# Kernel optimization log

Hardware: AMD Instinct MI355X
Metric: run time of the kernel (lower is better)

Reference implementation:

```python
import jax, jax.numpy as jnp
import numpy as np

N, D_IN, D_OUT, A, B = 100000, 128, 64, 8, 512
F = 2 * D_OUT  # feature_dim = output_dim * 2


def setup_inputs() -> dict:
    key = jax.random.key(0)
    ks = jax.random.split(key, 6)
    x = jax.random.normal(ks[0], (N, D_IN), jnp.float32)
    batch = jnp.sort(jax.random.randint(ks[1], (N,), 0, B)).astype(jnp.int32)
    def lin(k, out_d, in_d):
        return jax.random.normal(k, (out_d, in_d), jnp.float32) / np.float32(np.sqrt(in_d))
    W_in = lin(ks[2], F, D_IN)
    b_in = jnp.zeros((F,), jnp.float32)
    W_a = lin(ks[3], A, F)
    b_a = jnp.zeros((A,), jnp.float32)
    h_dim = 2 * F * A + D_IN + F
    W_out = lin(ks[4], D_OUT, h_dim)
    b_out = jnp.zeros((D_OUT,), jnp.float32)
    return {"x": x, "batch": batch, "num_segments": B,
            "W_in": W_in, "b_in": b_in, "W_a": W_a, "b_a": b_a,
            "W_out": W_out, "b_out": b_out}


def reference(x, batch, num_segments, W_in, b_in, W_a, b_a, W_out, b_out):
    # transform_in
    xp = x @ W_in.T + b_in                          # [N, F]
    # aggregator_activation('potential') = exp(-|.|)
    score = jnp.exp(-jnp.abs(xp @ W_a.T + b_a))     # [N, A]
    # einsum('nf,na->afn') materialized as [N, A, F] (node-major for segment ops)
    e = score[:, :, None] * xp[:, None, :]          # [N, A, F]
    seg_sum = jax.ops.segment_sum(e, batch, num_segments=num_segments)      # [B, A, F]
    counts = jax.ops.segment_sum(jnp.ones((e.shape[0], 1, 1), e.dtype), batch,
                                 num_segments=num_segments)                  # [B, 1, 1]
    mean_p = seg_sum / jnp.maximum(counts, 1.0)
    max_p = jax.ops.segment_max(e, batch, num_segments=num_segments)        # [B, A, F]
    max_p = jnp.where(counts > 0, max_p, 0.0)
    # cat along feature dim then flatten (A, 2F) -> matches torch transpose+cat+reshape
    agg = jnp.concatenate([mean_p, max_p], axis=-1).reshape(num_segments, -1)  # [B, 2*F*A]
    H = jnp.concatenate([x, xp, agg[batch]], axis=-1)  # [N, D_IN + F + 2*F*A]
    return jax.nn.relu(H @ W_out.T + b_out)            # [N, D_OUT]
```

## Files before the change

### kernel.cpp

```cpp
#include <hip/hip_runtime.h>
#include <math.h>

#define N_NODES 100000
#define D_INPUT 128
#define FDIM 128
#define A_HEADS 8
#define B_SEGS 512
#define D_OUTPUT 64
#define H_DIM 2304

typedef __attribute__((ext_vector_type(8))) __bf16 bf16x8;
typedef __attribute__((ext_vector_type(4))) float f32x4;

static __device__ inline unsigned short f2bfu(float f) {
    unsigned u = __builtin_bit_cast(unsigned, f);
    u += 0x7fffu + ((u >> 16) & 1u);
    return (unsigned short)(u >> 16);
}
static __device__ inline unsigned packbf(float a, float b) {
    return (unsigned)f2bfu(a) | ((unsigned)f2bfu(b) << 16);
}
static __device__ inline float bfl(unsigned u) {
    unsigned x = u << 16; return __builtin_bit_cast(float, x);
}
static __device__ inline float bfh(unsigned u) {
    unsigned x = u & 0xffff0000u; return __builtin_bit_cast(float, x);
}
static __device__ inline bf16x8 pack8(float4 a, float4 b) {
    union { unsigned u[4]; bf16x8 v; } r;
    r.u[0] = packbf(a.x, a.y); r.u[1] = packbf(a.z, a.w);
    r.u[2] = packbf(b.x, b.y); r.u[3] = packbf(b.z, b.w);
    return r.v;
}

__global__ void seg_bounds_kernel(const int* __restrict__ batch, int n,
                                  int* __restrict__ seg_start) {
    int b = threadIdx.x;
    if (b > B_SEGS) return;
    int lo = 0, hi = n;
    while (lo < hi) {
        int mid = (lo + hi) >> 1;
        if (batch[mid] < b) lo = mid + 1; else hi = mid;
    }
    seg_start[b] = lo;
}

__global__ __launch_bounds__(512, 2) void mega_kernel(
        const float* __restrict__ x, const int* __restrict__ seg_start,
        const float* __restrict__ W_in, const float* __restrict__ b_in,
        const float* __restrict__ W_a, const float* __restrict__ b_a,
        const float* __restrict__ W_out, const float* __restrict__ b_out,
        unsigned short* __restrict__ out_part, float* __restrict__ agg_proj) {
    __shared__ __align__(16) unsigned WbL[128 * 68];
    __shared__ __align__(16) unsigned WoL[64 * 132];
    __shared__ __align__(16) unsigned WaL[16 * 68];
    __shared__ __align__(16) unsigned XP[128 * 68];
    __shared__ float scoref[128 * 8];
    unsigned short* XPs = (unsigned short*)XP;
    float* XPf = (float*)XP;

    const int b = blockIdx.x;
    const int start = seg_start[b], end = seg_start[b + 1];
    const int cnt = end - start;
    const int t = threadIdx.x;

    if (cnt == 0) {
        if (t < 64) agg_proj[b * 64 + t] = b_out[t];
        return;
    }

#pragma unroll
    for (int i = 0; i < 16; ++i) {
        int idx = i * 512 + t, row = idx >> 6, c = idx & 63;
        float2 v = *(const float2*)(W_in + (size_t)row * 128 + c * 2);
        WbL[row * 68 + c] = packbf(v.x, v.y);
    }
#pragma unroll
    for (int i = 0; i < 16; ++i) {
        int idx = i * 512 + t, row = idx >> 7, c = idx & 127;
        float2 v = *(const float2*)(W_out + (size_t)row * H_DIM + c * 2);
        WoL[row * 132 + c] = packbf(v.x, v.y);
    }
    {
        int row = t >> 6, c = t & 63;
        float2 v = *(const float2*)(W_a + (size_t)row * 128 + c * 2);
        WaL[row * 68 + c] = packbf(v.x, v.y);
        WaL[(row + 8) * 68 + c] = 0u;
    }
    __syncthreads();

    const int w = t >> 6, l = t & 63, lr = l & 15, lk = l >> 4;
    const int a0 = t >> 6;
    const int f2 = t & 63;

    const f32x4 z4 = {0.f, 0.f, 0.f, 0.f};
    float sum0 = 0.f, sum1 = 0.f, mx0 = -INFINITY, mx1 = -INFINITY;

    for (int c0 = start; c0 < end; c0 += 128) {
        const int rc = min(128, end - c0);
        const int arow = c0 + w * 16 + lr;
        const int arowc = min(arow, end - 1);

        bf16x8 af[4];
#pragma unroll
        for (int ks = 0; ks < 4; ++ks) {
            const float4* xp4 = (const float4*)(x + (size_t)arowc * 128 + ks * 32 + lk * 8);
            af[ks] = pack8(xp4[0], xp4[1]);
        }
        f32x4 acc[8];
#pragma unroll
        for (int nr = 0; nr < 8; ++nr) acc[nr] = z4;
#pragma unroll
        for (int ks = 0; ks < 4; ++ks)
#pragma unroll
            for (int nr = 0; nr < 8; ++nr) {
                bf16x8 bfrag = *(const bf16x8*)&WbL[(nr * 16 + lr) * 68 + ks * 16 + lk * 4];
                acc[nr] = __builtin_amdgcn_mfma_f32_16x16x32_bf16(af[ks], bfrag, acc[nr], 0, 0, 0);
            }
#pragma unroll
        for (int nr = 0; nr < 8; ++nr) {
            float bf = b_in[nr * 16 + lr];
#pragma unroll
            for (int r = 0; r < 4; ++r) {
                int row = w * 16 + lk * 4 + r;
                XPs[row * 136 + nr * 16 + lr] = f2bfu(((const float*)&acc[nr])[r] + bf);
            }
        }
        bf16x8 xf[4];
#pragma unroll
        for (int ks = 0; ks < 4; ++ks)
            xf[ks] = *(const bf16x8*)&XPs[(w * 16 + lr) * 136 + ks * 32 + lk * 8];
        f32x4 sacc = z4;
#pragma unroll
        for (int ks = 0; ks < 4; ++ks) {
            bf16x8 bfrag = *(const bf16x8*)&WaL[lr * 68 + ks * 16 + lk * 4];
            sacc = __builtin_amdgcn_mfma_f32_16x16x32_bf16(xf[ks], bfrag, sacc, 0, 0, 0);
        }
        if (lr < A_HEADS) {
            float ba = b_a[lr];
#pragma unroll
            for (int r = 0; r < 4; ++r) {
                int row = w * 16 + lk * 4 + r;
                scoref[row * 8 + lr] = __expf(-fabsf(((const float*)&sacc)[r] + ba));
            }
        }
        f32x4 aco[4];
#pragma unroll
        for (int nr = 0; nr < 4; ++nr) aco[nr] = z4;
#pragma unroll
        for (int ks = 0; ks < 4; ++ks)
#pragma unroll
            for (int nr = 0; nr < 4; ++nr) {
                bf16x8 b0 = *(const bf16x8*)&WoL[(nr * 16 + lr) * 132 + ks * 16 + lk * 4];
                aco[nr] = __builtin_amdgcn_mfma_f32_16x16x32_bf16(af[ks], b0, aco[nr], 0, 0, 0);
                bf16x8 b1 = *(const bf16x8*)&WoL[(nr * 16 + lr) * 132 + 64 + ks * 16 + lk * 4];
                aco[nr] = __builtin_amdgcn_mfma_f32_16x16x32_bf16(xf[ks], b1, aco[nr], 0, 0, 0);
            }
#pragma unroll
        for (int nr = 0; nr < 4; ++nr)
#pragma unroll
            for (int r = 0; r < 4; ++r) {
                int n = c0 + w * 16 + lk * 4 + r;
                if (n < end)
                    out_part[(size_t)n * 64 + nr * 16 + lr] = f2bfu(((const float*)&aco[nr])[r]);
            }
        __syncthreads();

        for (int i = 0; i < rc; ++i) {
            unsigned u = XP[i * 68 + f2];
            float sa = scoref[i * 8 + a0];
            float e0 = sa * bfl(u), e1 = sa * bfh(u);
            sum0 += e0; sum1 += e1;
            mx0 = fmaxf(mx0, e0); mx1 = fmaxf(mx1, e1);
        }
        __syncthreads();
    }

    const float inv = 1.f / (float)cnt;
    XPf[a0 * 256 + 2 * f2]       = sum0 * inv;
    XPf[a0 * 256 + 2 * f2 + 1]   = sum1 * inv;
    XPf[a0 * 256 + 128 + 2 * f2]     = mx0;
    XPf[a0 * 256 + 128 + 2 * f2 + 1] = mx1;
    __syncthreads();

#pragma unroll
    for (int i = 0; i < 8; ++i) {
        int o = w * 8 + i;
        const float* wrow = W_out + (size_t)o * H_DIM + 256;
        float partial = 0.f;
#pragma unroll
        for (int c = 0; c < 8; ++c) {
            int jj = c * 256 + l * 4;
            float4 wv = *(const float4*)&wrow[jj];
            float4 av = *(const float4*)&XPf[jj];
            partial = fmaf(wv.x, av.x, partial);
            partial = fmaf(wv.y, av.y, partial);
            partial = fmaf(wv.z, av.z, partial);
            partial = fmaf(wv.w, av.w, partial);
        }
#pragma unroll
        for (int m = 1; m < 64; m <<= 1) partial += __shfl_xor(partial, m);
        if (l == 0) agg_proj[b * D_OUTPUT + o] = partial + b_out[o];
    }
}

__global__ __launch_bounds__(256) void out_final_kernel(
        const unsigned* __restrict__ out_part, const int* __restrict__ batch,
        const float* __restrict__ agg_proj, float* __restrict__ out) {
    int q = blockIdx.x * 256 + threadIdx.x;
    if (q >= N_NODES * 16) return;
    int n = q >> 4, c4 = (q & 15) * 4;
    int bs = batch[n];
    uint2 v = *(const uint2*)(out_part + (size_t)n * 32 + (c4 >> 1));
    float4 ap = *(const float4*)(agg_proj + (size_t)bs * 64 + c4);
    float4 o;
    o.x = fmaxf(bfl(v.x) + ap.x, 0.f);
    o.y = fmaxf(bfh(v.x) + ap.y, 0.f);
    o.z = fmaxf(bfl(v.y) + ap.z, 0.f);
    o.w = fmaxf(bfh(v.y) + ap.w, 0.f);
    *(float4*)(out + (size_t)n * 64 + c4) = o;
}

extern "C" void kernel_launch(void* const* d_in, const int* in_sizes, int n_in,
                              void* d_out, int out_size, void* d_ws, size_t ws_size,
                              hipStream_t stream) {
    const float* x     = (const float*)d_in[0];
    const int*   batch = (const int*)d_in[1];
    const float* W_in  = (const float*)d_in[3];
    const float* b_in  = (const float*)d_in[4];
    const float* W_a   = (const float*)d_in[5];
    const float* b_a   = (const float*)d_in[6];
    const float* W_out = (const float*)d_in[7];
    const float* b_out = (const float*)d_in[8];
    float* out = (float*)d_out;

    float* agg_proj = (float*)d_ws;
    int* seg_start = (int*)(agg_proj + B_SEGS * D_OUTPUT);
    unsigned short* out_part = (unsigned short*)(seg_start + 520);
    unsigned* out_part_u32 = (unsigned*)out_part;

    seg_bounds_kernel<<<1, 1024, 0, stream>>>(batch, N_NODES, seg_start);
    mega_kernel<<<B_SEGS, 512, 0, stream>>>(
        x, seg_start, W_in, b_in, W_a, b_a, W_out, b_out, out_part, agg_proj);
    out_final_kernel<<<(N_NODES * 16 + 255) / 256, 256, 0, stream>>>(
        out_part_u32, batch, agg_proj, out);
}
```

Baseline: 71.87 us.

## Split segments across two blocks, pre-convert weights, move aggregation projection to separate kernel

Weight bf16 conversion moves into a one-time prepass kernel, so the main kernel reads bf16 weight fragments straight from global/L2 instead of staging them in LDS. Each segment is now handled by two 256-thread blocks that write partial sum/max buffers. A new kernel combines the halves and projects the aggregate through bf16 W_out weights. The inner aggregation loop is unrolled by two, with each thread covering two heads. This raises parallelism and cuts LDS use, at the cost of extra launches, partial-buffer traffic, and weight fragment loads from global memory inside the MFMA loop.

```diff
diff --git a/kernel.cpp b/kernel.cpp
--- a/kernel.cpp
+++ b/kernel.cpp
@@ -45,61 +45,71 @@
     seg_start[b] = lo;
 }
 
-__global__ __launch_bounds__(512, 2) void mega_kernel(
+__global__ __launch_bounds__(256) void wconv_kernel(
+        const float* __restrict__ W_in, const float* __restrict__ W_a,
+        const float* __restrict__ W_out, unsigned* __restrict__ Wb,
+        unsigned* __restrict__ Wa, unsigned* __restrict__ Wo,
+        unsigned* __restrict__ Wagg) {
+    int i = blockIdx.x * 256 + threadIdx.x;
+    if (i < 8192) {
+        float2 v = *(const float2*)(W_in + (size_t)i * 2);
+        Wb[i] = packbf(v.x, v.y);
+    } else if (i < 9216) {
+        int j = i - 8192;
+        if (j < 512) {
+            float2 v = *(const float2*)(W_a + (size_t)j * 2);
+            Wa[j] = packbf(v.x, v.y);
+        } else Wa[j] = 0u;
+    } else if (i < 17408) {
+        int j = i - 9216;
+        int row = j >> 7, cu = j & 127;
+        float2 v = *(const float2*)(W_out + (size_t)row * H_DIM + cu * 2);
+        Wo[j] = packbf(v.x, v.y);
+    } else if (i < 82944) {
+        int j = i - 17408;
+        int row = j >> 10, cu = j & 1023;
+        float2 v = *(const float2*)(W_out + (size_t)row * H_DIM + 256 + cu * 2);
+        Wagg[j] = packbf(v.x, v.y);
+    }
+}
+
+__global__ __launch_bounds__(256, 4) void mega_kernel(
         const float* __restrict__ x, const int* __restrict__ seg_start,
-        const float* __restrict__ W_in, const float* __restrict__ b_in,
-        const float* __restrict__ W_a, const float* __restrict__ b_a,
-        const float* __restrict__ W_out, const float* __restrict__ b_out,
-        unsigned short* __restrict__ out_part, float* __restrict__ agg_proj) {
-    __shared__ __align__(16) unsigned WbL[128 * 68];
-    __shared__ __align__(16) unsigned WoL[64 * 132];
-    __shared__ __align__(16) unsigned WaL[16 * 68];
-    __shared__ __align__(16) unsigned XP[128 * 68];
-    __shared__ float scoref[128 * 8];
+        const float* __restrict__ b_in, const float* __restrict__ b_a,
+        const unsigned* __restrict__ Wb, const unsigned* __restrict__ Wa,
+        const unsigned* __restrict__ Wo, unsigned short* __restrict__ out_part,
+        float* __restrict__ psum, float* __restrict__ pmax) {
+    __shared__ __align__(16) unsigned XP[64 * 68];
+    __shared__ float scoref[64 * 8];
     unsigned short* XPs = (unsigned short*)XP;
-    float* XPf = (float*)XP;
-
-    const int b = blockIdx.x;
-    const int start = seg_start[b], end = seg_start[b + 1];
-    const int cnt = end - start;
+
+    const int bb = blockIdx.x;
+    const int seg = bb >> 1, half = bb & 1;
+    const int s0 = seg_start[seg], s1 = seg_start[seg + 1];
+    const int cnt = s1 - s0;
+    const int h = (cnt + 1) >> 1;
+    const int hstart = s0 + half * h;
+    const int hend = min(s1, hstart + h);
+
     const int t = threadIdx.x;
-
-    if (cnt == 0) {
-        if (t < 64) agg_proj[b * 64 + t] = b_out[t];
-        return;
-    }
-
-#pragma unroll
-    for (int i = 0; i < 16; ++i) {
-        int idx = i * 512 + t, row = idx >> 6, c = idx & 63;
-        float2 v = *(const float2*)(W_in + (size_t)row * 128 + c * 2);
-        WbL[row * 68 + c] = packbf(v.x, v.y);
-    }
-#pragma unroll
-    for (int i = 0; i < 16; ++i) {
-        int idx = i * 512 + t, row = idx >> 7, c = idx & 127;
-        float2 v = *(const float2*)(W_out + (size_t)row * H_DIM + c * 2);
-        WoL[row * 132 + c] = packbf(v.x, v.y);
-    }
-    {
-        int row = t >> 6, c = t & 63;
-        float2 v = *(const float2*)(W_a + (size_t)row * 128 + c * 2);
-        WaL[row * 68 + c] = packbf(v.x, v.y);
-        WaL[(row + 8) * 68 + c] = 0u;
-    }
-    __syncthreads();
-
     const int w = t >> 6, l = t & 63, lr = l & 15, lk = l >> 4;
-    const int a0 = t >> 6;
-    const int f2 = t & 63;
+    const int a0 = t >> 6, f2 = t & 63;
+
+    float binv[8];
+#pragma unroll
+    for (int nr = 0; nr < 8; ++nr) binv[nr] = b_in[nr * 16 + lr];
+    const float ba = b_a[lr & 7];
 
     const f32x4 z4 = {0.f, 0.f, 0.f, 0.f};
-    float sum0 = 0.f, sum1 = 0.f, mx0 = -INFINITY, mx1 = -INFINITY;
-
-    for (int c0 = start; c0 < end; c0 += 128) {
-        const int rc = min(128, end - c0);
+    float sum0a = 0.f, sum1a = 0.f, sum2a = 0.f, sum3a = 0.f;
+    float sum0b = 0.f, sum1b = 0.f, sum2b = 0.f, sum3b = 0.f;
+    float mx0a = -INFINITY, mx1a = -INFINITY, mx2a = -INFINITY, mx3a = -INFINITY;
+    float mx0b = -INFINITY, mx1b = -INFINITY, mx2b = -INFINITY, mx3b = -INFINITY;
+
+    for (int c0 = hstart; c0 < hend; c0 += 64) {
+        const int rc = min(64, hend - c0);
         const int arow = c0 + w * 16 + lr;
-        const int arowc = min(arow, end - 1);
+        const int arowc = min(arow, hend - 1);
 
         bf16x8 af[4];
 #pragma unroll
@@ -114,18 +124,16 @@
         for (int ks = 0; ks < 4; ++ks)
 #pragma unroll
             for (int nr = 0; nr < 8; ++nr) {
-                bf16x8 bfrag = *(const bf16x8*)&WbL[(nr * 16 + lr) * 68 + ks * 16 + lk * 4];
+                bf16x8 bfrag = *(const bf16x8*)&Wb[(nr * 16 + lr) * 64 + ks * 16 + lk * 4];
                 acc[nr] = __builtin_amdgcn_mfma_f32_16x16x32_bf16(af[ks], bfrag, acc[nr], 0, 0, 0);
             }
 #pragma unroll
-        for (int nr = 0; nr < 8; ++nr) {
-            float bf = b_in[nr * 16 + lr];
+        for (int nr = 0; nr < 8; ++nr)
 #pragma unroll
             for (int r = 0; r < 4; ++r) {
                 int row = w * 16 + lk * 4 + r;
-                XPs[row * 136 + nr * 16 + lr] = f2bfu(((const float*)&acc[nr])[r] + bf);
-            }
-        }
+                XPs[row * 136 + nr * 16 + lr] = f2bfu(((const float*)&acc[nr])[r] + binv[nr]);
+            }
         bf16x8 xf[4];
 #pragma unroll
         for (int ks = 0; ks < 4; ++ks)
@@ -133,11 +141,10 @@
         f32x4 sacc = z4;
 #pragma unroll
         for (int ks = 0; ks < 4; ++ks) {
-            bf16x8 bfrag = *(const bf16x8*)&WaL[lr * 68 + ks * 16 + lk * 4];
+            bf16x8 bfrag = *(const bf16x8*)&Wa[lr * 64 + ks * 16 + lk * 4];
             sacc = __builtin_amdgcn_mfma_f32_16x16x32_bf16(xf[ks], bfrag, sacc, 0, 0, 0);
         }
         if (lr < A_HEADS) {
-            float ba = b_a[lr];
 #pragma unroll
             for (int r = 0; r < 4; ++r) {
                 int row = w * 16 + lk * 4 + r;
@@ -151,9 +158,9 @@
         for (int ks = 0; ks < 4; ++ks)
 #pragma unroll
             for (int nr = 0; nr < 4; ++nr) {
-                bf16x8 b0 = *(const bf16x8*)&WoL[(nr * 16 + lr) * 132 + ks * 16 + lk * 4];
+                bf16x8 b0 = *(const bf16x8*)&Wo[(nr * 16 + lr) * 128 + ks * 16 + lk * 4];
                 aco[nr] = __builtin_amdgcn_mfma_f32_16x16x32_bf16(af[ks], b0, aco[nr], 0, 0, 0);
-                bf16x8 b1 = *(const bf16x8*)&WoL[(nr * 16 + lr) * 132 + 64 + ks * 16 + lk * 4];
+                bf16x8 b1 = *(const bf16x8*)&Wo[(nr * 16 + lr) * 128 + 64 + ks * 16 + lk * 4];
                 aco[nr] = __builtin_amdgcn_mfma_f32_16x16x32_bf16(xf[ks], b1, aco[nr], 0, 0, 0);
             }
 #pragma unroll
@@ -161,46 +168,91 @@
 #pragma unroll
             for (int r = 0; r < 4; ++r) {
                 int n = c0 + w * 16 + lk * 4 + r;
-                if (n < end)
+                if (n < hend)
                     out_part[(size_t)n * 64 + nr * 16 + lr] = f2bfu(((const float*)&aco[nr])[r]);
             }
         __syncthreads();
 
-        for (int i = 0; i < rc; ++i) {
-            unsigned u = XP[i * 68 + f2];
-            float sa = scoref[i * 8 + a0];
-            float e0 = sa * bfl(u), e1 = sa * bfh(u);
-            sum0 += e0; sum1 += e1;
-            mx0 = fmaxf(mx0, e0); mx1 = fmaxf(mx1, e1);
+        int i = 0;
+        for (; i + 1 < rc; i += 2) {
+            unsigned u0 = XP[i * 68 + f2];
+            unsigned u1 = XP[(i + 1) * 68 + f2];
+            float sA0 = scoref[i * 8 + a0],       sB0 = scoref[i * 8 + a0 + 4];
+            float sA1 = scoref[(i + 1) * 8 + a0], sB1 = scoref[(i + 1) * 8 + a0 + 4];
+            float x00 = bfl(u0), x01 = bfh(u0);
+            float x10 = bfl(u1), x11 = bfh(u1);
+            float e;
+            e = sA0 * x00; sum0a += e; mx0a = fmaxf(mx0a, e);
+            e = sA0 * x01; sum1a += e; mx1a = fmaxf(mx1a, e);
+            e = sB0 * x00; sum2a += e; mx2a = fmaxf(mx2a, e);
+            e = sB0 * x01; sum3a += e; mx3a = fmaxf(mx3a, e);
+            e = sA1 * x10; sum0b += e; mx0b = fmaxf(mx0b, e);
+            e = sA1 * x11; sum1b += e; mx1b = fmaxf(mx1b, e);
+            e = sB1 * x10; sum2b += e; mx2b = fmaxf(mx2b, e);
+            e = sB1 * x11; sum3b += e; mx3b = fmaxf(mx3b, e);
+        }
+        if (i < rc) {
+            unsigned u0 = XP[i * 68 + f2];
+            float sA0 = scoref[i * 8 + a0], sB0 = scoref[i * 8 + a0 + 4];
+            float x00 = bfl(u0), x01 = bfh(u0);
+            float e;
+            e = sA0 * x00; sum0a += e; mx0a = fmaxf(mx0a, e);
+            e = sA0 * x01; sum1a += e; mx1a = fmaxf(mx1a, e);
+            e = sB0 * x00; sum2a += e; mx2a = fmaxf(mx2a, e);
+            e = sB0 * x01; sum3a += e; mx3a = fmaxf(mx3a, e);
         }
         __syncthreads();
     }
 
-    const float inv = 1.f / (float)cnt;
-    XPf[a0 * 256 + 2 * f2]       = sum0 * inv;
-    XPf[a0 * 256 + 2 * f2 + 1]   = sum1 * inv;
-    XPf[a0 * 256 + 128 + 2 * f2]     = mx0;
-    XPf[a0 * 256 + 128 + 2 * f2 + 1] = mx1;
+    float* ps = psum + (size_t)bb * 1024;
+    float* pm = pmax + (size_t)bb * 1024;
+    *(float2*)&ps[a0 * 128 + 2 * f2]       = make_float2(sum0a + sum0b, sum1a + sum1b);
+    *(float2*)&ps[(a0 + 4) * 128 + 2 * f2] = make_float2(sum2a + sum2b, sum3a + sum3b);
+    *(float2*)&pm[a0 * 128 + 2 * f2]       = make_float2(fmaxf(mx0a, mx0b), fmaxf(mx1a, mx1b));
+    *(float2*)&pm[(a0 + 4) * 128 + 2 * f2] = make_float2(fmaxf(mx2a, mx2b), fmaxf(mx3a, mx3b));
+}
+
+__global__ __launch_bounds__(256) void seg_final_kernel(
+        const float* __restrict__ psum, const float* __restrict__ pmax,
+        const int* __restrict__ seg_start, const unsigned* __restrict__ Wagg,
+        const float* __restrict__ b_out, float* __restrict__ agg_proj) {
+    __shared__ float agg[2048];
+    const int b = blockIdx.x, t = threadIdx.x;
+    const int cnt = seg_start[b + 1] - seg_start[b];
+    const float inv = (cnt > 0) ? 1.f / (float)cnt : 0.f;
+#pragma unroll
+    for (int i = 0; i < 4; ++i) {
+        int idx = i * 256 + t;
+        float s = psum[(size_t)(2 * b) * 1024 + idx] + psum[(size_t)(2 * b + 1) * 1024 + idx];
+        float m = fmaxf(pmax[(size_t)(2 * b) * 1024 + idx], pmax[(size_t)(2 * b + 1) * 1024 + idx]);
+        int a = idx >> 7, f = idx & 127;
+        agg[a * 256 + f] = s * inv;
+        agg[a * 256 + 128 + f] = (cnt > 0) ? m : 0.f;
+    }
     __syncthreads();
-
-#pragma unroll
-    for (int i = 0; i < 8; ++i) {
-        int o = w * 8 + i;
-        const float* wrow = W_out + (size_t)o * H_DIM + 256;
+    const int wave = t >> 6, lane = t & 63;
+#pragma unroll
+    for (int i = 0; i < 16; ++i) {
+        int o = wave * 16 + i;
+        const unsigned* wrow = Wagg + (size_t)o * 1024;
         float partial = 0.f;
 #pragma unroll
-        for (int c = 0; c < 8; ++c) {
-            int jj = c * 256 + l * 4;
-            float4 wv = *(const float4*)&wrow[jj];
-            float4 av = *(const float4*)&XPf[jj];
-            partial = fmaf(wv.x, av.x, partial);
-            partial = fmaf(wv.y, av.y, partial);
-            partial = fmaf(wv.z, av.z, partial);
-            partial = fmaf(wv.w, av.w, partial);
+        for (int c = 0; c < 4; ++c) {
+            int j4 = c * 256 + lane * 4;
+            uint4 wv = *(const uint4*)&wrow[j4];
+            const float* av = &agg[2 * j4];
+            partial = fmaf(bfl(wv.x), av[0], partial);
+            partial = fmaf(bfh(wv.x), av[1], partial);
+            partial = fmaf(bfl(wv.y), av[2], partial);
+            partial = fmaf(bfh(wv.y), av[3], partial);
+            partial = fmaf(bfl(wv.z), av[4], partial);
+            partial = fmaf(bfh(wv.z), av[5], partial);
+            partial = fmaf(bfl(wv.w), av[6], partial);
+            partial = fmaf(bfh(wv.w), av[7], partial);
         }
 #pragma unroll
         for (int m = 1; m < 64; m <<= 1) partial += __shfl_xor(partial, m);
-        if (l == 0) agg_proj[b * D_OUTPUT + o] = partial + b_out[o];
+        if (lane == 0) agg_proj[b * D_OUTPUT + o] = partial + b_out[o];
     }
 }
 
@@ -235,13 +287,22 @@
     float* out = (float*)d_out;
 
     float* agg_proj = (float*)d_ws;
-    int* seg_start = (int*)(agg_proj + B_SEGS * D_OUTPUT);
-    unsigned short* out_part = (unsigned short*)(seg_start + 520);
+    int* seg_start  = (int*)(agg_proj + 32768);
+    unsigned* Wb    = (unsigned*)(seg_start + 520);
+    unsigned* Wa    = Wb + 8192;
+    unsigned* Wo    = Wa + 1024;
+    unsigned* Wagg  = Wo + 8192;
+    float* psum     = (float*)(Wagg + 65536);
+    float* pmax     = psum + 1048576;
+    unsigned short* out_part = (unsigned short*)(pmax + 1048576);
     unsigned* out_part_u32 = (unsigned*)out_part;
 
     seg_bounds_kernel<<<1, 1024, 0, stream>>>(batch, N_NODES, seg_start);
-    mega_kernel<<<B_SEGS, 512, 0, stream>>>(
-        x, seg_start, W_in, b_in, W_a, b_a, W_out, b_out, out_part, agg_proj);
+    wconv_kernel<<<324, 256, 0, stream>>>(W_in, W_a, W_out, Wb, Wa, Wo, Wagg);
+    mega_kernel<<<2 * B_SEGS, 256, 0, stream>>>(
+        x, seg_start, b_in, b_a, Wb, Wa, Wo, out_part, psum, pmax);
+    seg_final_kernel<<<B_SEGS, 256, 0, stream>>>(
+        psum, pmax, seg_start, Wagg, b_out, agg_proj);
     out_final_kernel<<<(N_NODES * 16 + 255) / 256, 256, 0, stream>>>(
         out_part_u32, batch, agg_proj, out);
 }
```

After: 225.0 us. +213.1%, slower.

## Pre-convert weights to bf16 once and fuse final output pass into segment kernel

Applied to the files above, without the earlier changes.

Adds a small kernel that converts W_in, W_a and W_out to bf16 once, so each segment block copies ready-made bf16 weights instead of converting fp32 itself. The W_out tile for the node term is now read straight from global/L2 rather than staged in LDS, and the aggregate projection uses bf16 weights. The separate output kernel is removed: each block applies bias plus ReLU to its own segment's rows after computing the projection. Together with the lower LDS use and launch bounds of 4 blocks per CU, this aims to raise occupancy and cut launches. The cost is one extra launch and more global weight traffic inside the inner loop.

```diff
diff --git a/kernel.cpp b/kernel.cpp
--- a/kernel.cpp
+++ b/kernel.cpp
@@ -45,61 +45,87 @@
     seg_start[b] = lo;
 }
 
-__global__ __launch_bounds__(512, 2) void mega_kernel(
+__global__ __launch_bounds__(256) void wconv_kernel(
+        const float* __restrict__ W_in, const float* __restrict__ W_a,
+        const float* __restrict__ W_out, unsigned* __restrict__ Wb,
+        unsigned* __restrict__ Wa, unsigned* __restrict__ Wo,
+        unsigned* __restrict__ Wagg) {
+    int i = blockIdx.x * 256 + threadIdx.x;
+    if (i < 8192) {
+        float2 v = *(const float2*)(W_in + (size_t)i * 2);
+        Wb[i] = packbf(v.x, v.y);
+    } else if (i < 9216) {
+        int j = i - 8192;
+        if (j < 512) {
+            float2 v = *(const float2*)(W_a + (size_t)j * 2);
+            Wa[j] = packbf(v.x, v.y);
+        } else Wa[j] = 0u;
+    } else if (i < 17408) {
+        int j = i - 9216;
+        int row = j >> 7, cu = j & 127;
+        float2 v = *(const float2*)(W_out + (size_t)row * H_DIM + cu * 2);
+        Wo[j] = packbf(v.x, v.y);
+    } else if (i < 82944) {
+        int j = i - 17408;
+        int row = j >> 10, cu = j & 1023;
+        float2 v = *(const float2*)(W_out + (size_t)row * H_DIM + 256 + cu * 2);
+        Wagg[j] = packbf(v.x, v.y);
+    }
+}
+
+__global__ __launch_bounds__(512, 4) void mega_kernel(
         const float* __restrict__ x, const int* __restrict__ seg_start,
-        const float* __restrict__ W_in, const float* __restrict__ b_in,
-        const float* __restrict__ W_a, const float* __restrict__ b_a,
-        const float* __restrict__ W_out, const float* __restrict__ b_out,
-        unsigned short* __restrict__ out_part, float* __restrict__ agg_proj) {
+        const float* __restrict__ b_in, const float* __restrict__ b_a,
+        const float* __restrict__ b_out, const unsigned* __restrict__ Wb,
+        const unsigned* __restrict__ Wa, const unsigned* __restrict__ Wo,
+        const unsigned* __restrict__ Wagg, unsigned* __restrict__ out_part_u32,
+        float* __restrict__ out) {
     __shared__ __align__(16) unsigned WbL[128 * 68];
-    __shared__ __align__(16) unsigned WoL[64 * 132];
     __shared__ __align__(16) unsigned WaL[16 * 68];
     __shared__ __align__(16) unsigned XP[128 * 68];
     __shared__ float scoref[128 * 8];
+    __shared__ float projL[64];
     unsigned short* XPs = (unsigned short*)XP;
     float* XPf = (float*)XP;
+    unsigned short* opart16 = (unsigned short*)out_part_u32;
 
     const int b = blockIdx.x;
-    const int start = seg_start[b], end = seg_start[b + 1];
-    const int cnt = end - start;
+    const int s0 = seg_start[b], s1 = seg_start[b + 1];
+    const int cnt = s1 - s0;
+    if (cnt == 0) return;
     const int t = threadIdx.x;
 
-    if (cnt == 0) {
-        if (t < 64) agg_proj[b * 64 + t] = b_out[t];
-        return;
-    }
-
-#pragma unroll
-    for (int i = 0; i < 16; ++i) {
-        int idx = i * 512 + t, row = idx >> 6, c = idx & 63;
-        float2 v = *(const float2*)(W_in + (size_t)row * 128 + c * 2);
-        WbL[row * 68 + c] = packbf(v.x, v.y);
-    }
-#pragma unroll
-    for (int i = 0; i < 16; ++i) {
-        int idx = i * 512 + t, row = idx >> 7, c = idx & 127;
-        float2 v = *(const float2*)(W_out + (size_t)row * H_DIM + c * 2);
-        WoL[row * 132 + c] = packbf(v.x, v.y);
-    }
     {
-        int row = t >> 6, c = t & 63;
-        float2 v = *(const float2*)(W_a + (size_t)row * 128 + c * 2);
-        WaL[row * 68 + c] = packbf(v.x, v.y);
-        WaL[(row + 8) * 68 + c] = 0u;
+        const uint4* src = (const uint4*)Wb;
+#pragma unroll
+        for (int i = 0; i < 4; ++i) {
+            int idx = i * 512 + t;
+            int row = idx >> 4, c4 = idx & 15;
+            *(uint4*)&WbL[row * 68 + c4 * 4] = src[idx];
+        }
+        if (t < 256) {
+            const uint4* sa = (const uint4*)Wa;
+            int row = t >> 4, c4 = t & 15;
+            *(uint4*)&WaL[row * 68 + c4 * 4] = sa[t];
+        }
     }
     __syncthreads();
 
     const int w = t >> 6, l = t & 63, lr = l & 15, lk = l >> 4;
-    const int a0 = t >> 6;
-    const int f2 = t & 63;
+    const int a0 = w, f2 = l;
+
+    float binv[8];
+#pragma unroll
+    for (int nr = 0; nr < 8; ++nr) binv[nr] = b_in[nr * 16 + lr];
+    const float ba = b_a[lr & 7];
 
     const f32x4 z4 = {0.f, 0.f, 0.f, 0.f};
     float sum0 = 0.f, sum1 = 0.f, mx0 = -INFINITY, mx1 = -INFINITY;
 
-    for (int c0 = start; c0 < end; c0 += 128) {
-        const int rc = min(128, end - c0);
+    for (int c0 = s0; c0 < s1; c0 += 128) {
+        const int rc = min(128, s1 - c0);
         const int arow = c0 + w * 16 + lr;
-        const int arowc = min(arow, end - 1);
+        const int arowc = min(arow, s1 - 1);
 
         bf16x8 af[4];
 #pragma unroll
@@ -118,14 +144,12 @@
                 acc[nr] = __builtin_amdgcn_mfma_f32_16x16x32_bf16(af[ks], bfrag, acc[nr], 0, 0, 0);
             }
 #pragma unroll
-        for (int nr = 0; nr < 8; ++nr) {
-            float bf = b_in[nr * 16 + lr];
+        for (int nr = 0; nr < 8; ++nr)
 #pragma unroll
             for (int r = 0; r < 4; ++r) {
                 int row = w * 16 + lk * 4 + r;
-                XPs[row * 136 + nr * 16 + lr] = f2bfu(((const float*)&acc[nr])[r] + bf);
-            }
-        }
+                XPs[row * 136 + nr * 16 + lr] = f2bfu(((const float*)&acc[nr])[r] + binv[nr]);
+            }
         bf16x8 xf[4];
 #pragma unroll
         for (int ks = 0; ks < 4; ++ks)
@@ -137,7 +161,6 @@
             sacc = __builtin_amdgcn_mfma_f32_16x16x32_bf16(xf[ks], bfrag, sacc, 0, 0, 0);
         }
         if (lr < A_HEADS) {
-            float ba = b_a[lr];
 #pragma unroll
             for (int r = 0; r < 4; ++r) {
                 int row = w * 16 + lk * 4 + r;
@@ -151,9 +174,9 @@
         for (int ks = 0; ks < 4; ++ks)
 #pragma unroll
             for (int nr = 0; nr < 4; ++nr) {
-                bf16x8 b0 = *(const bf16x8*)&WoL[(nr * 16 + lr) * 132 + ks * 16 + lk * 4];
+                bf16x8 b0 = *(const bf16x8*)&Wo[(nr * 16 + lr) * 128 + ks * 16 + lk * 4];
                 aco[nr] = __builtin_amdgcn_mfma_f32_16x16x32_bf16(af[ks], b0, aco[nr], 0, 0, 0);
-                bf16x8 b1 = *(const bf16x8*)&WoL[(nr * 16 + lr) * 132 + 64 + ks * 16 + lk * 4];
+                bf16x8 b1 = *(const bf16x8*)&Wo[(nr * 16 + lr) * 128 + 64 + ks * 16 + lk * 4];
                 aco[nr] = __builtin_amdgcn_mfma_f32_16x16x32_bf16(xf[ks], b1, aco[nr], 0, 0, 0);
             }
 #pragma unroll
@@ -161,8 +184,8 @@
 #pragma unroll
             for (int r = 0; r < 4; ++r) {
                 int n = c0 + w * 16 + lk * 4 + r;
-                if (n < end)
-                    out_part[(size_t)n * 64 + nr * 16 + lr] = f2bfu(((const float*)&aco[nr])[r]);
+                if (n < s1)
+                    opart16[(size_t)n * 64 + nr * 16 + lr] = f2bfu(((const float*)&aco[nr])[r]);
             }
         __syncthreads();
 
@@ -177,8 +200,8 @@
     }
 
     const float inv = 1.f / (float)cnt;
-    XPf[a0 * 256 + 2 * f2]       = sum0 * inv;
-    XPf[a0 * 256 + 2 * f2 + 1]   = sum1 * inv;
+    XPf[a0 * 256 + 2 * f2]           = sum0 * inv;
+    XPf[a0 * 256 + 2 * f2 + 1]       = sum1 * inv;
     XPf[a0 * 256 + 128 + 2 * f2]     = mx0;
     XPf[a0 * 256 + 128 + 2 * f2 + 1] = mx1;
     __syncthreads();
@@ -186,39 +209,50 @@
 #pragma unroll
     for (int i = 0; i < 8; ++i) {
         int o = w * 8 + i;
-        const float* wrow = W_out + (size_t)o * H_DIM + 256;
+        const unsigned* wrow = Wagg + (size_t)o * 1024;
         float partial = 0.f;
 #pragma unroll
-        for (int c = 0; c < 8; ++c) {
-            int jj = c * 256 + l * 4;
-            float4 wv = *(const float4*)&wrow[jj];
-            float4 av = *(const float4*)&XPf[jj];
-            partial = fmaf(wv.x, av.x, partial);
-            partial = fmaf(wv.y, av.y, partial);
-            partial = fmaf(wv.z, av.z, partial);
-            partial = fmaf(wv.w, av.w, partial);
+        for (int c = 0; c < 4; ++c) {
+            int j4 = c * 256 + l * 4;
+            uint4 wv = *(const uint4*)&wrow[j4];
+            const float* av = &XPf[2 * j4];
+            partial = fmaf(bfl(wv.x), av[0], partial);
+            partial = fmaf(bfh(wv.x), av[1], partial);
+            partial = fmaf(bfl(wv.y), av[2], partial);
+            partial = fmaf(bfh(wv.y), av[3], partial);
+            partial = fmaf(bfl(wv.z), av[4], partial);
+            partial = fmaf(bfh(wv.z), av[5], partial);
+            partial = fmaf(bfl(wv.w), av[6], partial);
+            partial = fmaf(bfh(wv.w), av[7], partial);
         }
 #pragma unroll
         for (int m = 1; m < 64; m <<= 1) partial += __shfl_xor(partial, m);
-        if (l == 0) agg_proj[b * D_OUTPUT + o] = partial + b_out[o];
-    }
-}
-
-__global__ __launch_bounds__(256) void out_final_kernel(
-        const unsigned* __restrict__ out_part, const int* __restrict__ batch,
-        const float* __restrict__ agg_proj, float* __restrict__ out) {
-    int q = blockIdx.x * 256 + threadIdx.x;
-    if (q >= N_NODES * 16) return;
-    int n = q >> 4, c4 = (q & 15) * 4;
-    int bs = batch[n];
-    uint2 v = *(const uint2*)(out_part + (size_t)n * 32 + (c4 >> 1));
-    float4 ap = *(const float4*)(agg_proj + (size_t)bs * 64 + c4);
-    float4 o;
-    o.x = fmaxf(bfl(v.x) + ap.x, 0.f);
-    o.y = fmaxf(bfh(v.x) + ap.y, 0.f);
-    o.z = fmaxf(bfl(v.y) + ap.z, 0.f);
-    o.w = fmaxf(bfh(v.y) + ap.w, 0.f);
-    *(float4*)(out + (size_t)n * 64 + c4) = o;
+        if (l == 0) projL[o] = partial + b_out[o];
+    }
+    __threadfence_block();
+    __syncthreads();
+
+    const int rr = t >> 3, cg = t & 7;
+    float p[8];
+#pragma unroll
+    for (int j = 0; j < 8; ++j) p[j] = projL[cg * 8 + j];
+    for (int r0 = s0; r0 < s1; r0 += 64) {
+        int row = r0 + rr;
+        if (row < s1) {
+            uint4 v = *(const uint4*)&out_part_u32[(size_t)row * 32 + cg * 4];
+            float4 o0, o1;
+            o0.x = fmaxf(bfl(v.x) + p[0], 0.f);
+            o0.y = fmaxf(bfh(v.x) + p[1], 0.f);
+            o0.z = fmaxf(bfl(v.y) + p[2], 0.f);
+            o0.w = fmaxf(bfh(v.y) + p[3], 0.f);
+            o1.x = fmaxf(bfl(v.z) + p[4], 0.f);
+            o1.y = fmaxf(bfh(v.z) + p[5], 0.f);
+            o1.z = fmaxf(bfl(v.w) + p[6], 0.f);
+            o1.w = fmaxf(bfh(v.w) + p[7], 0.f);
+            *(float4*)&out[(size_t)row * 64 + cg * 8] = o0;
+            *(float4*)&out[(size_t)row * 64 + cg * 8 + 4] = o1;
+        }
+    }
 }
 
 extern "C" void kernel_launch(void* const* d_in, const int* in_sizes, int n_in,
@@ -234,14 +268,15 @@
     const float* b_out = (const float*)d_in[8];
     float* out = (float*)d_out;
 
-    float* agg_proj = (float*)d_ws;
-    int* seg_start = (int*)(agg_proj + B_SEGS * D_OUTPUT);
-    unsigned short* out_part = (unsigned short*)(seg_start + 520);
-    unsigned* out_part_u32 = (unsigned*)out_part;
+    int* seg_start  = (int*)d_ws;
+    unsigned* Wb    = (unsigned*)(seg_start + 520);
+    unsigned* Wa    = Wb + 8192;
+    unsigned* Wo    = Wa + 1024;
+    unsigned* Wagg  = Wo + 8192;
+    unsigned* out_part_u32 = Wagg + 65536;
 
     seg_bounds_kernel<<<1, 1024, 0, stream>>>(batch, N_NODES, seg_start);
+    wconv_kernel<<<324, 256, 0, stream>>>(W_in, W_a, W_out, Wb, Wa, Wo, Wagg);
     mega_kernel<<<B_SEGS, 512, 0, stream>>>(
-        x, seg_start, W_in, b_in, W_a, b_a, W_out, b_out, out_part, agg_proj);
-    out_final_kernel<<<(N_NODES * 16 + 255) / 256, 256, 0, stream>>>(
-        out_part_u32, batch, agg_proj, out);
-}
+        x, seg_start, b_in, b_a, b_out, Wb, Wa, Wo, Wagg, out_part_u32, out);
+}
```

Measured after the change: 93.98 us. 30.8% more time.
